# Performance work log

Hardware: AMD Instinct MI355X
Metric: run time of the kernel (lower is better)

The kernel has to match this reference:

```python
import jax, jax.numpy as jnp
import numpy as np

BS1, BS2, NUM_EC = 32, 128, 64
CONV_DIM, MEM_DIM, MLP_DIM = 64, 256, 256
Q_DIM = 4 * CONV_DIM  # query_dim of criteria


def setup_inputs() -> dict:
    key = jax.random.key(0)
    k = jax.random.split(key, 6)
    in_dim = Q_DIM + MEM_DIM
    s_a = 1.0 / np.sqrt(in_dim)
    return {
        "ehr_vector": jax.random.normal(k[0], (BS2, MEM_DIM), dtype=jnp.float32),
        "criteria": jax.random.normal(k[1], (BS1, NUM_EC, Q_DIM), dtype=jnp.float32),
        "ec_mask": jnp.ones((BS1, NUM_EC), dtype=jnp.float32),
        # alignment: Linear(mem_dim + 4*conv_dim, 1) -> store as [in_dim] vector + scalar bias
        "W_align": jax.random.normal(k[2], (in_dim,), dtype=jnp.float32) * s_a,
        "b_align": jax.random.normal(k[3], (1,), dtype=jnp.float32) * s_a,
        # mlp: Linear(mem_dim + 4*conv_dim, mlp_dim) -> store as [in_dim, mlp_dim]
        "W_mlp": jax.random.normal(k[4], (in_dim, MLP_DIM), dtype=jnp.float32) * s_a,
        "b_mlp": jax.random.normal(k[5], (MLP_DIM,), dtype=jnp.float32) * s_a,
    }


def reference(ehr_vector, criteria, ec_mask, W_align, b_align, W_mlp, b_mlp):
    # Math identical to: att = softmax(Linear(cat[criteria, ehr]), dim=ec);
    # h = Linear_mlp(cat[criteria, ehr] * att). Concat is never materialized:
    # split both linear weights along the input dim instead.
    q = criteria.shape[-1]
    Wa_c, Wa_e = W_align[:q], W_align[q:]
    # additive attention logits: [bs1, bs2, num_ec]
    logit_c = jnp.einsum("beq,q->be", criteria, Wa_c)      # [bs1, num_ec]
    logit_e = jnp.einsum("pm,m->p", ehr_vector, Wa_e)      # [bs2]
    logits = logit_c[:, None, :] + logit_e[None, :, None] + b_align[0]
    att = jax.nn.softmax(logits, axis=2)                   # softmax over num_ec

    Wm_c, Wm_e = W_mlp[:q], W_mlp[q:]
    proj_c = jnp.einsum("beq,qd->bed", criteria, Wm_c)     # [bs1, num_ec, mlp]
    proj_e = jnp.einsum("pm,md->pd", ehr_vector, Wm_e)     # [bs2, mlp]
    # mlp((cat * att)) = att * (cat @ W_mlp) + b_mlp  (att is scalar per (b,p,e))
    h = att[..., None] * (proj_c[:, None, :, :] + proj_e[None, :, None, :]) + b_mlp
    return h  # [bs1, bs2, num_ec, mlp_dim]
```

## Files before the change

### kernel.cpp

```cpp
#include <hip/hip_runtime.h>

#define BS1 32
#define BS2 128
#define NEC 64
#define QD  256
#define MD  256

__global__ __launch_bounds__(64)
void att_kernel(const float* __restrict__ crit,
                const float* __restrict__ w_align,
                float* __restrict__ att) {
    __shared__ float wa[QD];
    int b = blockIdx.x, e = threadIdx.x;
    for (int i = e; i < QD; i += 64) wa[i] = w_align[i];
    __syncthreads();
    const float* row = crit + (b * NEC + e) * QD;
    float acc = 0.f;
    for (int k = 0; k < QD; k += 4) {
        float4 u = *(const float4*)(row + k);
        acc = fmaf(u.x, wa[k + 0], acc);
        acc = fmaf(u.y, wa[k + 1], acc);
        acc = fmaf(u.z, wa[k + 2], acc);
        acc = fmaf(u.w, wa[k + 3], acc);
    }
    float m = acc;
    #pragma unroll
    for (int off = 32; off; off >>= 1) m = fmaxf(m, __shfl_xor(m, off));
    float ex = __expf(acc - m);
    float s = ex;
    #pragma unroll
    for (int off = 32; off; off >>= 1) s += __shfl_xor(s, off);
    att[b * NEC + e] = ex / s;
}

__global__ __launch_bounds__(256)
void gemm_rows8(const float* __restrict__ A,
                const float* __restrict__ B,
                float* __restrict__ out) {
    __shared__ float As[8 * QD];
    int tid = threadIdx.x;
    int m0 = blockIdx.x * 8;
    {
        const float* src = A + m0 * QD + tid * 8;
        float4 a0 = *(const float4*)src;
        float4 a1 = *(const float4*)(src + 4);
        *(float4*)&As[tid * 8]     = a0;
        *(float4*)&As[tid * 8 + 4] = a1;
    }
    __syncthreads();
    int r = tid >> 5;
    int c = (tid & 31) * 8;
    float acc[8] = {0.f,0.f,0.f,0.f,0.f,0.f,0.f,0.f};
    #pragma unroll 4
    for (int k = 0; k < QD; ++k) {
        float a = As[r * QD + k];
        const float* bp = B + k * MD + c;
        float4 b0 = *(const float4*)bp;
        float4 b1 = *(const float4*)(bp + 4);
        acc[0] = fmaf(a, b0.x, acc[0]);
        acc[1] = fmaf(a, b0.y, acc[1]);
        acc[2] = fmaf(a, b0.z, acc[2]);
        acc[3] = fmaf(a, b0.w, acc[3]);
        acc[4] = fmaf(a, b1.x, acc[4]);
        acc[5] = fmaf(a, b1.y, acc[5]);
        acc[6] = fmaf(a, b1.z, acc[6]);
        acc[7] = fmaf(a, b1.w, acc[7]);
    }
    float* o = out + (m0 + r) * MD + c;
    *(float4*)o       = make_float4(acc[0], acc[1], acc[2], acc[3]);
    *(float4*)(o + 4) = make_float4(acc[4], acc[5], acc[6], acc[7]);
}

__global__ __launch_bounds__(256)
void final_kernel(const float* __restrict__ att,
                  const float* __restrict__ proj_c,
                  const float* __restrict__ proj_e,
                  const float* __restrict__ b_mlp,
                  float*       __restrict__ out) {
    __shared__ float pe[MD], bm[MD], attb[NEC];
    int tid = threadIdx.x;
    int bp  = blockIdx.x;
    int b = bp >> 7, p = bp & 127;
    pe[tid] = proj_e[p * MD + tid];
    bm[tid] = b_mlp[tid];
    if (tid < NEC) attb[tid] = att[b * NEC + tid];
    __syncthreads();
    const float* pc_base = proj_c + b * NEC * MD;
    float* out_base = out + (size_t)bp * (NEC * MD);
    #pragma unroll
    for (int pass = 0; pass < 8; ++pass) {
        int idx = pass * 256 + tid;
        int e = idx >> 5;
        int d = (idx & 31) * 8;
        float a = attb[e];
        const float* pc = pc_base + e * MD + d;
        float4 c0 = *(const float4*)pc;
        float4 c1 = *(const float4*)(pc + 4);
        float4 e0 = *(const float4*)&pe[d];
        float4 e1 = *(const float4*)&pe[d + 4];
        float4 m0 = *(const float4*)&bm[d];
        float4 m1 = *(const float4*)&bm[d + 4];
        float4 r0, r1;
        r0.x = fmaf(a, c0.x + e0.x, m0.x);
        r0.y = fmaf(a, c0.y + e0.y, m0.y);
        r0.z = fmaf(a, c0.z + e0.z, m0.z);
        r0.w = fmaf(a, c0.w + e0.w, m0.w);
        r1.x = fmaf(a, c1.x + e1.x, m1.x);
        r1.y = fmaf(a, c1.y + e1.y, m1.y);
        r1.z = fmaf(a, c1.z + e1.z, m1.z);
        r1.w = fmaf(a, c1.w + e1.w, m1.w);
        float* o = out_base + (size_t)idx * 8;
        *(float4*)o       = r0;
        *(float4*)(o + 4) = r1;
    }
}

extern "C" void kernel_launch(void* const* d_in, const int* in_sizes, int n_in,
                              void* d_out, int out_size, void* d_ws, size_t ws_size,
                              hipStream_t stream) {
    const float* ehr     = (const float*)d_in[0];
    const float* crit    = (const float*)d_in[1];
    const float* w_align = (const float*)d_in[3];
    const float* w_mlp   = (const float*)d_in[5];
    const float* b_mlp   = (const float*)d_in[6];
    float* out = (float*)d_out;

    float* att    = (float*)d_ws;
    float* proj_c = att + BS1 * NEC;
    float* proj_e = proj_c + BS1 * NEC * MD;

    att_kernel<<<BS1, 64, 0, stream>>>(crit, w_align, att);
    gemm_rows8<<<(BS1 * NEC) / 8, 256, 0, stream>>>(crit, w_mlp, proj_c);
    gemm_rows8<<<BS2 / 8, 256, 0, stream>>>(ehr, w_mlp + QD * MD, proj_e);
    final_kernel<<<BS1 * BS2, 256, 0, stream>>>(att, proj_c, proj_e, b_mlp, out);
}
```

Before: 349.6 us.

## Fuse attention and both projection GEMMs into one prep kernel; nontemporal final stores

```diff
diff --git a/kernel.cpp b/kernel.cpp
--- a/kernel.cpp
+++ b/kernel.cpp
@@ -6,69 +6,86 @@
 #define QD  256
 #define MD  256
 
-__global__ __launch_bounds__(64)
-void att_kernel(const float* __restrict__ crit,
-                const float* __restrict__ w_align,
-                float* __restrict__ att) {
-    __shared__ float wa[QD];
-    int b = blockIdx.x, e = threadIdx.x;
-    for (int i = e; i < QD; i += 64) wa[i] = w_align[i];
-    __syncthreads();
-    const float* row = crit + (b * NEC + e) * QD;
-    float acc = 0.f;
-    for (int k = 0; k < QD; k += 4) {
-        float4 u = *(const float4*)(row + k);
-        acc = fmaf(u.x, wa[k + 0], acc);
-        acc = fmaf(u.y, wa[k + 1], acc);
-        acc = fmaf(u.z, wa[k + 2], acc);
-        acc = fmaf(u.w, wa[k + 3], acc);
-    }
-    float m = acc;
-    #pragma unroll
-    for (int off = 32; off; off >>= 1) m = fmaxf(m, __shfl_xor(m, off));
-    float ex = __expf(acc - m);
-    float s = ex;
-    #pragma unroll
-    for (int off = 32; off; off >>= 1) s += __shfl_xor(s, off);
-    att[b * NEC + e] = ex / s;
-}
+typedef float fx4 __attribute__((ext_vector_type(4)));
 
 __global__ __launch_bounds__(256)
-void gemm_rows8(const float* __restrict__ A,
-                const float* __restrict__ B,
-                float* __restrict__ out) {
-    __shared__ float As[8 * QD];
+void prep_kernel(const float* __restrict__ crit,
+                 const float* __restrict__ ehr,
+                 const float* __restrict__ w_mlp,
+                 const float* __restrict__ w_align,
+                 float* __restrict__ proj_c,
+                 float* __restrict__ proj_e,
+                 float* __restrict__ att) {
+    __shared__ float smem[8 * QD];
+    __shared__ float logits[NEC];
     int tid = threadIdx.x;
-    int m0 = blockIdx.x * 8;
-    {
-        const float* src = A + m0 * QD + tid * 8;
-        float4 a0 = *(const float4*)src;
-        float4 a1 = *(const float4*)(src + 4);
-        *(float4*)&As[tid * 8]     = a0;
-        *(float4*)&As[tid * 8 + 4] = a1;
+    int blk = blockIdx.x;
+
+    if (blk < 272) {
+        const float* A; const float* B; float* out; int m0;
+        if (blk < 256) { A = crit; B = w_mlp;           out = proj_c; m0 = blk * 8; }
+        else           { A = ehr;  B = w_mlp + QD * MD; out = proj_e; m0 = (blk - 256) * 8; }
+        {
+            const float* src = A + m0 * QD + tid * 8;
+            float4 a0 = *(const float4*)src;
+            float4 a1 = *(const float4*)(src + 4);
+            *(float4*)&smem[tid * 8]     = a0;
+            *(float4*)&smem[tid * 8 + 4] = a1;
+        }
+        __syncthreads();
+        int r = tid >> 5;
+        int c = (tid & 31) * 8;
+        float acc[8] = {0.f,0.f,0.f,0.f,0.f,0.f,0.f,0.f};
+        #pragma unroll 4
+        for (int k = 0; k < QD; ++k) {
+            float a = smem[r * QD + k];
+            const float* bp = B + k * MD + c;
+            float4 b0 = *(const float4*)bp;
+            float4 b1 = *(const float4*)(bp + 4);
+            acc[0] = fmaf(a, b0.x, acc[0]);
+            acc[1] = fmaf(a, b0.y, acc[1]);
+            acc[2] = fmaf(a, b0.z, acc[2]);
+            acc[3] = fmaf(a, b0.w, acc[3]);
+            acc[4] = fmaf(a, b1.x, acc[4]);
+            acc[5] = fmaf(a, b1.y, acc[5]);
+            acc[6] = fmaf(a, b1.z, acc[6]);
+            acc[7] = fmaf(a, b1.w, acc[7]);
+        }
+        float* o = out + (m0 + r) * MD + c;
+        *(float4*)o       = make_float4(acc[0], acc[1], acc[2], acc[3]);
+        *(float4*)(o + 4) = make_float4(acc[4], acc[5], acc[6], acc[7]);
+    } else {
+        int b = blk - 272;
+        smem[tid] = w_align[tid];
+        __syncthreads();
+        int e = tid >> 2, q = tid & 3;
+        const float* row = crit + (b * NEC + e) * QD + q * 64;
+        const float* w   = &smem[q * 64];
+        float acc = 0.f;
+        #pragma unroll
+        for (int k = 0; k < 64; k += 4) {
+            float4 u = *(const float4*)(row + k);
+            acc = fmaf(u.x, w[k + 0], acc);
+            acc = fmaf(u.y, w[k + 1], acc);
+            acc = fmaf(u.z, w[k + 2], acc);
+            acc = fmaf(u.w, w[k + 3], acc);
+        }
+        acc += __shfl_xor(acc, 1);
+        acc += __shfl_xor(acc, 2);
+        if (q == 0) logits[e] = acc;
+        __syncthreads();
+        if (tid < NEC) {
+            float l = logits[tid];
+            float m = l;
+            #pragma unroll
+            for (int off = 32; off; off >>= 1) m = fmaxf(m, __shfl_xor(m, off));
+            float ex = __expf(l - m);
+            float s = ex;
+            #pragma unroll
+            for (int off = 32; off; off >>= 1) s += __shfl_xor(s, off);
+            att[b * NEC + tid] = ex / s;
+        }
     }
-    __syncthreads();
-    int r = tid >> 5;
-    int c = (tid & 31) * 8;
-    float acc[8] = {0.f,0.f,0.f,0.f,0.f,0.f,0.f,0.f};
-    #pragma unroll 4
-    for (int k = 0; k < QD; ++k) {
-        float a = As[r * QD + k];
-        const float* bp = B + k * MD + c;
-        float4 b0 = *(const float4*)bp;
-        float4 b1 = *(const float4*)(bp + 4);
-        acc[0] = fmaf(a, b0.x, acc[0]);
-        acc[1] = fmaf(a, b0.y, acc[1]);
-        acc[2] = fmaf(a, b0.z, acc[2]);
-        acc[3] = fmaf(a, b0.w, acc[3]);
-        acc[4] = fmaf(a, b1.x, acc[4]);
-        acc[5] = fmaf(a, b1.y, acc[5]);
-        acc[6] = fmaf(a, b1.z, acc[6]);
-        acc[7] = fmaf(a, b1.w, acc[7]);
-    }
-    float* o = out + (m0 + r) * MD + c;
-    *(float4*)o       = make_float4(acc[0], acc[1], acc[2], acc[3]);
-    *(float4*)(o + 4) = make_float4(acc[4], acc[5], acc[6], acc[7]);
 }
 
 __global__ __launch_bounds__(256)
@@ -77,41 +94,42 @@
                   const float* __restrict__ proj_e,
                   const float* __restrict__ b_mlp,
                   float*       __restrict__ out) {
-    __shared__ float pe[MD], bm[MD], attb[NEC];
     int tid = threadIdx.x;
     int bp  = blockIdx.x;
     int b = bp >> 7, p = bp & 127;
-    pe[tid] = proj_e[p * MD + tid];
-    bm[tid] = b_mlp[tid];
-    if (tid < NEC) attb[tid] = att[b * NEC + tid];
-    __syncthreads();
-    const float* pc_base = proj_c + b * NEC * MD;
-    float* out_base = out + (size_t)bp * (NEC * MD);
+    int wid = tid >> 5;
+    int d   = (tid & 31) * 8;
+
+    const float4 e0 = *(const float4*)(proj_e + p * MD + d);
+    const float4 e1 = *(const float4*)(proj_e + p * MD + d + 4);
+    const float4 m0 = *(const float4*)(b_mlp + d);
+    const float4 m1 = *(const float4*)(b_mlp + d + 4);
+
+    const float* attp = att + b * NEC + wid;
+    float a[8];
+    #pragma unroll
+    for (int pass = 0; pass < 8; ++pass) a[pass] = attp[pass * 8];
+
+    const float* pc = proj_c + (b * NEC + wid) * MD + d;
+    float*       o  = out + (size_t)bp * (NEC * MD) + tid * 8;
+
     #pragma unroll
     for (int pass = 0; pass < 8; ++pass) {
-        int idx = pass * 256 + tid;
-        int e = idx >> 5;
-        int d = (idx & 31) * 8;
-        float a = attb[e];
-        const float* pc = pc_base + e * MD + d;
         float4 c0 = *(const float4*)pc;
         float4 c1 = *(const float4*)(pc + 4);
-        float4 e0 = *(const float4*)&pe[d];
-        float4 e1 = *(const float4*)&pe[d + 4];
-        float4 m0 = *(const float4*)&bm[d];
-        float4 m1 = *(const float4*)&bm[d + 4];
-        float4 r0, r1;
-        r0.x = fmaf(a, c0.x + e0.x, m0.x);
-        r0.y = fmaf(a, c0.y + e0.y, m0.y);
-        r0.z = fmaf(a, c0.z + e0.z, m0.z);
-        r0.w = fmaf(a, c0.w + e0.w, m0.w);
-        r1.x = fmaf(a, c1.x + e1.x, m1.x);
-        r1.y = fmaf(a, c1.y + e1.y, m1.y);
-        r1.z = fmaf(a, c1.z + e1.z, m1.z);
-        r1.w = fmaf(a, c1.w + e1.w, m1.w);
-        float* o = out_base + (size_t)idx * 8;
-        *(float4*)o       = r0;
-        *(float4*)(o + 4) = r1;
+        fx4 r0, r1;
+        r0.x = fmaf(a[pass], c0.x + e0.x, m0.x);
+        r0.y = fmaf(a[pass], c0.y + e0.y, m0.y);
+        r0.z = fmaf(a[pass], c0.z + e0.z, m0.z);
+        r0.w = fmaf(a[pass], c0.w + e0.w, m0.w);
+        r1.x = fmaf(a[pass], c1.x + e1.x, m1.x);
+        r1.y = fmaf(a[pass], c1.y + e1.y, m1.y);
+        r1.z = fmaf(a[pass], c1.z + e1.z, m1.z);
+        r1.w = fmaf(a[pass], c1.w + e1.w, m1.w);
+        __builtin_nontemporal_store(r0, (fx4*)o);
+        __builtin_nontemporal_store(r1, (fx4*)(o + 4));
+        pc += 8 * MD;
+        o  += 256 * 8;
     }
 }
 
@@ -129,8 +147,7 @@
     float* proj_c = att + BS1 * NEC;
     float* proj_e = proj_c + BS1 * NEC * MD;
 
-    att_kernel<<<BS1, 64, 0, stream>>>(crit, w_align, att);
-    gemm_rows8<<<(BS1 * NEC) / 8, 256, 0, stream>>>(crit, w_mlp, proj_c);
-    gemm_rows8<<<BS2 / 8, 256, 0, stream>>>(ehr, w_mlp + QD * MD, proj_e);
+    prep_kernel<<<272 + BS1, 256, 0, stream>>>(crit, ehr, w_mlp, w_align,
+                                               proj_c, proj_e, att);
     final_kernel<<<BS1 * BS2, 256, 0, stream>>>(att, proj_c, proj_e, b_mlp, out);
 }
```

New measurement: 376.2 us. 1.08x slower.
